# Optimization experiments

Hardware: AMD Instinct MI355X
Metric: run time of the kernel (lower is better)

## Reference

```python
import jax, jax.numpy as jnp
import numpy as np

N_NODES = 100000
N_EDGES = 1600000
DIM = 64
BN_EPS = 1e-5


def setup_inputs() -> dict:
    key = jax.random.key(0)
    ks = jax.random.split(key, 6)
    x = jax.random.normal(ks[0], (N_NODES, DIM), dtype=jnp.float32)
    edge_index = jax.random.randint(ks[1], (2, N_EDGES), 0, N_NODES, dtype=jnp.int32)
    W = jax.random.normal(ks[2], (DIM, DIM), dtype=jnp.float32) / np.sqrt(DIM)
    b = jax.random.normal(ks[3], (DIM,), dtype=jnp.float32) * 0.01
    gamma = jnp.ones((DIM,), dtype=jnp.float32)
    beta = jnp.zeros((DIM,), dtype=jnp.float32)
    return {"x": x, "edge_index": edge_index, "W": W, "b": b, "gamma": gamma, "beta": beta}


def reference(x, edge_index, W, b, gamma, beta):
    n = x.shape[0]
    src, dst = edge_index[0], edge_index[1]
    # GCNConv adds self loops
    loop = jnp.arange(n, dtype=edge_index.dtype)
    src = jnp.concatenate([src, loop])
    dst = jnp.concatenate([dst, loop])
    # symmetric degree normalization: D^-1/2 (A+I) D^-1/2
    deg = jax.ops.segment_sum(jnp.ones(src.shape[0], x.dtype), dst, num_segments=n)
    dinv = jnp.where(deg > 0, jax.lax.rsqrt(deg), 0.0)
    norm = dinv[src] * dinv[dst]  # [E+N]
    h = x @ W  # [N, D] transform before aggregation (GCN order)
    msg = h[src] * norm[:, None]  # gather + scale
    out = jax.ops.segment_sum(msg, dst, num_segments=n) + b  # scatter-add
    # BatchNorm1d (training mode: batch statistics, biased variance)
    mean = jnp.mean(out, axis=0)
    var = jnp.mean(jnp.square(out - mean), axis=0)
    out = (out - mean) * jax.lax.rsqrt(var + BN_EPS) * gamma + beta
    # ReLU; dropout is identity in eval mode
    return jax.nn.relu(out)
```

## Files before the change

kernel.cpp:

```cpp
#include <hip/hip_runtime.h>

#define N_NODES 100000
#define N_EDGES 1600000
#define DIM 64
#define BN_EPS 1e-5f

#define BNODES 128
#define NBUCK ((N_NODES + BNODES - 1) / BNODES)
#define CAP_RAW 2560
#define CAP_OUT 3584
#define TILE 4096
#define ABLK ((N_EDGES + TILE - 1) / TILE)
#define DUMMY N_NODES

#define GBLK 6250

typedef __bf16 bf16x8 __attribute__((ext_vector_type(8)));
typedef float floatx4 __attribute__((ext_vector_type(4)));

static __device__ __forceinline__ unsigned short f2bf(float f) {
    unsigned u = __float_as_uint(f);
    u = (u + 0x7FFFu + ((u >> 16) & 1u)) >> 16;
    return (unsigned short)u;
}
static __device__ __forceinline__ float bf2f(unsigned short h) {
    return __uint_as_float(((unsigned)h) << 16);
}

__global__ void __launch_bounds__(1024)
passA_kernel(const int* __restrict__ src, const int* __restrict__ dst,
             int* __restrict__ cur, unsigned int* __restrict__ entries, int E) {
    __shared__ int hist[NBUCK];
    __shared__ int lbase[NBUCK];
    int t = threadIdx.x;
    if (t < NBUCK) hist[t] = 0;
    __syncthreads();

    int e0   = blockIdx.x * TILE;
    int eend = min(e0 + TILE, E);

    int dreg[4], sreg[4], ne = 0;
    for (int e = e0 + t; e < eend; e += 1024) {
        dreg[ne] = dst[e];
        sreg[ne] = src[e];
        atomicAdd(&hist[dreg[ne] >> 7], 1);
        ++ne;
    }
    __syncthreads();
    if (t < NBUCK) {
        int ii = t + (blockIdx.x * 331) % NBUCK;
        if (ii >= NBUCK) ii -= NBUCK;
        int c = hist[ii];
        lbase[ii] = (c > 0) ? atomicAdd(&cur[ii], c) : 0;
        hist[ii] = 0;
    }
    __syncthreads();
    for (int k = 0; k < ne; ++k) {
        int s = sreg[k];
        int d = dreg[k];
        int b = d >> 7;
        int r = atomicAdd(&hist[b], 1);
        int pos = lbase[b] + r;
        if (pos < CAP_RAW)
            entries[(size_t)b * CAP_OUT + pos] = ((unsigned)s << 7) | (unsigned)(d & 127);
    }
}

__global__ void passB1_kernel(unsigned int* __restrict__ entries, const int* __restrict__ cur,
                              int* __restrict__ rowbeg, int* __restrict__ rowend,
                              float* __restrict__ dinv, int N) {
    __shared__ unsigned int raw[CAP_RAW];
    __shared__ int hist[BNODES];
    __shared__ int sbuf[BNODES];
    __shared__ int startx[BNODES];
    __shared__ int cursor[BNODES];
    int bucket = blockIdx.x;
    int t = threadIdx.x;
    int node0 = bucket * BNODES;
    int nn = min(BNODES, N - node0);
    int cnt = min(cur[bucket], CAP_RAW);
    unsigned int* eb = entries + (size_t)bucket * CAP_OUT;

    if (t < BNODES) hist[t] = 0;
    __syncthreads();
    for (int i = t; i < cnt; i += 256) {
        unsigned int e = eb[i];
        raw[i] = e;
        atomicAdd(&hist[e & 127], 1);
    }
    __syncthreads();
    int pdeg_t = 0;
    if (t < BNODES) { pdeg_t = (hist[t] + 7) & ~7; sbuf[t] = pdeg_t; }
    __syncthreads();
    for (int off = 1; off < BNODES; off <<= 1) {
        int add = (t < BNODES && t >= off) ? sbuf[t - off] : 0;
        __syncthreads();
        if (t < BNODES) sbuf[t] += add;
        __syncthreads();
    }
    if (t < BNODES) {
        int ex = sbuf[t] - pdeg_t;
        startx[t] = ex;
        cursor[t] = ex;
    }
    __syncthreads();
    for (int i = t; i < cnt; i += 256) {
        unsigned int e = raw[i];
        int d = e & 127;
        int p = atomicAdd(&cursor[d], 1);
        eb[p] = e >> 7;
    }
    if (t < nn) {
        int dg  = hist[t];
        int pdg = (dg + 7) & ~7;
        int base = startx[t];
        for (int k = dg; k < pdg; ++k) eb[base + k] = DUMMY;
        int gbase = bucket * CAP_OUT + base;
        rowbeg[node0 + t] = gbase;
        rowend[node0 + t] = gbase + pdg;
        dinv[node0 + t]   = rsqrtf((float)(dg + 1));
    }
}

__global__ void __launch_bounds__(256)
gemm_kernel(const float* __restrict__ x, const float* __restrict__ W,
            const float* __restrict__ dinv, unsigned short* __restrict__ hb, int N) {
    int wave  = (blockIdx.x * blockDim.x + threadIdx.x) >> 6;
    int lane  = threadIdx.x & 63;
    int m     = lane & 15;
    int quad  = lane >> 4;

    bf16x8 bfrag[2][4];
#pragma unroll
    for (int c = 0; c < 2; ++c)
#pragma unroll
        for (int nt = 0; nt < 4; ++nt) {
            bf16x8 f;
#pragma unroll
            for (int j = 0; j < 8; ++j) {
                int k = c * 32 + quad * 8 + j;
                f[j] = (__bf16)W[k * DIM + nt * 16 + m];
            }
            bfrag[c][nt] = f;
        }

    int nchunks    = N >> 4;
    int totalwaves = (gridDim.x * blockDim.x) >> 6;
    for (int chunk = wave; chunk < nchunks; chunk += totalwaves) {
        int row0 = chunk * 16;
        const float* xr = x + (size_t)(row0 + m) * DIM;
        bf16x8 afrag[2];
#pragma unroll
        for (int c = 0; c < 2; ++c) {
            float4 lo = *(const float4*)(xr + c * 32 + quad * 8);
            float4 hi = *(const float4*)(xr + c * 32 + quad * 8 + 4);
            bf16x8 f;
            f[0] = (__bf16)lo.x; f[1] = (__bf16)lo.y; f[2] = (__bf16)lo.z; f[3] = (__bf16)lo.w;
            f[4] = (__bf16)hi.x; f[5] = (__bf16)hi.y; f[6] = (__bf16)hi.z; f[7] = (__bf16)hi.w;
            afrag[c] = f;
        }
        float dv[4];
#pragma unroll
        for (int r = 0; r < 4; ++r) dv[r] = dinv[row0 + quad * 4 + r];
#pragma unroll
        for (int nt = 0; nt < 4; ++nt) {
            floatx4 acc = {0.f, 0.f, 0.f, 0.f};
            acc = __builtin_amdgcn_mfma_f32_16x16x32_bf16(afrag[0], bfrag[0][nt], acc, 0, 0, 0);
            acc = __builtin_amdgcn_mfma_f32_16x16x32_bf16(afrag[1], bfrag[1][nt], acc, 0, 0, 0);
#pragma unroll
            for (int r = 0; r < 4; ++r) {
                int row = row0 + quad * 4 + r;
                hb[(size_t)row * DIM + nt * 16 + m] = f2bf(acc[r] * dv[r]);
            }
        }
    }
}

__global__ void __launch_bounds__(256)
gather_kernel(const int* __restrict__ rowbeg, const int* __restrict__ rowend,
              const unsigned int* __restrict__ srt, const unsigned short* __restrict__ hb,
              const float* __restrict__ dinv, float* __restrict__ out,
              float* __restrict__ partial, int N) {
    __shared__ float red[2][4][64];
    int lane = threadIdx.x & 63;
    int wv   = threadIdx.x >> 6;
    int g    = blockIdx.x * 4 + wv;
    int n0   = g << 2;
    float s_sum = 0.f, s_sq = 0.f;

    if (n0 < N) {
        int beg = __builtin_amdgcn_readfirstlane(rowbeg[n0]);
        int s1  = __builtin_amdgcn_readfirstlane(rowbeg[n0 + 1]);
        int s2  = __builtin_amdgcn_readfirstlane(rowbeg[n0 + 2]);
        int s3  = __builtin_amdgcn_readfirstlane(rowbeg[n0 + 3]);
        int end = __builtin_amdgcn_readfirstlane(rowend[n0 + 3]);
        float acc0 = 0.f, acc1 = 0.f, acc2 = 0.f, acc3 = 0.f;

        for (int base = beg; base < end; base += 64) {
            int idx = base + lane;
            unsigned int sv = (idx < end) ? srt[idx] : 0u;
            int cn = min(64, end - base);
            for (int j = 0; j < cn; j += 8) {
                int p0 = base + j;
                int k = (p0 >= s1) + (p0 >= s2) + (p0 >= s3);
                float v[8];
#pragma unroll
                for (int u = 0; u < 8; ++u) {
                    unsigned int s = (unsigned)__shfl((int)sv, j + u, 64);
                    v[u] = bf2f(hb[(size_t)s * DIM + lane]);
                }
                float csum = ((v[0] + v[1]) + (v[2] + v[3])) +
                             ((v[4] + v[5]) + (v[6] + v[7]));
                acc0 += (k == 0) ? csum : 0.f;
                acc1 += (k == 1) ? csum : 0.f;
                acc2 += (k == 2) ? csum : 0.f;
                acc3 += (k == 3) ? csum : 0.f;
            }
        }

        float v0 = (acc0 + bf2f(hb[(size_t)(n0 + 0) * DIM + lane])) * dinv[n0 + 0];
        float v1 = (acc1 + bf2f(hb[(size_t)(n0 + 1) * DIM + lane])) * dinv[n0 + 1];
        float v2 = (acc2 + bf2f(hb[(size_t)(n0 + 2) * DIM + lane])) * dinv[n0 + 2];
        float v3 = (acc3 + bf2f(hb[(size_t)(n0 + 3) * DIM + lane])) * dinv[n0 + 3];
        out[(size_t)(n0 + 0) * DIM + lane] = v0;
        out[(size_t)(n0 + 1) * DIM + lane] = v1;
        out[(size_t)(n0 + 2) * DIM + lane] = v2;
        out[(size_t)(n0 + 3) * DIM + lane] = v3;
        s_sum = ((v0 + v1) + (v2 + v3));
        s_sq  = ((v0 * v0 + v1 * v1) + (v2 * v2 + v3 * v3));
    }

    red[0][wv][lane] = s_sum;
    red[1][wv][lane] = s_sq;
    __syncthreads();
    if (threadIdx.x < 64) {
        int c = threadIdx.x;
        partial[(size_t)blockIdx.x * 128 + c] =
            red[0][0][c] + red[0][1][c] + red[0][2][c] + red[0][3][c];
        partial[(size_t)blockIdx.x * 128 + 64 + c] =
            red[1][0][c] + red[1][1][c] + red[1][2][c] + red[1][3][c];
    }
}

__global__ void reduce2_kernel(const float* __restrict__ partial, float* __restrict__ gstat) {
    __shared__ float buf[256];
    int t = threadIdx.x;
    int col = t & 127;
    int half = t >> 7;
    int r0 = blockIdx.x * 125;
    float acc = 0.f;
    for (int r = r0 + half; r < r0 + 125; r += 2)
        acc += partial[(size_t)r * 128 + col];
    buf[t] = acc;
    __syncthreads();
    if (t < 128) atomicAdd(&gstat[t], buf[t] + buf[t + 128]);
}

__global__ void bn_finalize_kernel(const float* __restrict__ gsum, const float* __restrict__ gsumsq,
                                   const float* __restrict__ gamma, const float* __restrict__ beta,
                                   float* __restrict__ scale, float* __restrict__ shift, int N) {
    int c = threadIdx.x;
    float invN = 1.0f / (float)N;
    float mean = gsum[c] * invN;
    float var  = gsumsq[c] * invN - mean * mean;
    float sc   = gamma[c] * rsqrtf(var + BN_EPS);
    scale[c] = sc;
    shift[c] = beta[c] - mean * sc;
}

__global__ void bn_apply_kernel(float4* __restrict__ out, const float* __restrict__ scale,
                                const float* __restrict__ shift, int total4) {
    int i = blockIdx.x * blockDim.x + threadIdx.x;
    if (i >= total4) return;
    int c = (i * 4) & 63;
    float4 v = out[i];
    float a0 = fmaf(v.x, scale[c],     shift[c]);
    float a1 = fmaf(v.y, scale[c + 1], shift[c + 1]);
    float a2 = fmaf(v.z, scale[c + 2], shift[c + 2]);
    float a3 = fmaf(v.w, scale[c + 3], shift[c + 3]);
    v.x = a0 > 0.f ? a0 : 0.f;
    v.y = a1 > 0.f ? a1 : 0.f;
    v.z = a2 > 0.f ? a2 : 0.f;
    v.w = a3 > 0.f ? a3 : 0.f;
    out[i] = v;
}

extern "C" void kernel_launch(void* const* d_in, const int* in_sizes, int n_in,
                              void* d_out, int out_size, void* d_ws, size_t ws_size,
                              hipStream_t stream) {
    const float* x     = (const float*)d_in[0];
    const int*   eidx  = (const int*)d_in[1];
    const float* W     = (const float*)d_in[2];
    const float* gamma = (const float*)d_in[4];
    const float* beta  = (const float*)d_in[5];
    float* out = (float*)d_out;

    const int N = N_NODES;
    const int E = N_EDGES;
    const int total = N * DIM;

    const int* src = eidx;
    const int* dst = eidx + E;

    unsigned short* hb = (unsigned short*)d_ws;
    float* dinv      = (float*)(hb + (size_t)(N + 1) * DIM);
    int*   rowbeg    = (int*)(dinv + N);
    int*   rowend    = rowbeg + N;
    int*   cur       = rowend + N;
    float* gsum      = (float*)(cur + NBUCK);
    float* gsumsq    = gsum + 64;
    float* scale     = gsumsq + 64;
    float* shift     = scale + 64;
    unsigned int* entries = (unsigned int*)(shift + 64);
    float* partial   = (float*)(entries + (size_t)NBUCK * CAP_OUT);

    hipMemsetAsync(cur, 0, (size_t)(NBUCK + 128) * sizeof(int), stream);
    hipMemsetAsync(hb + (size_t)N * DIM, 0, DIM * sizeof(unsigned short), stream);

    passA_kernel<<<ABLK, 1024, 0, stream>>>(src, dst, cur, entries, E);

    passB1_kernel<<<NBUCK, 256, 0, stream>>>(entries, cur, rowbeg, rowend, dinv, N);

    gemm_kernel<<<512, 256, 0, stream>>>(x, W, dinv, hb, N);

    gather_kernel<<<GBLK, 256, 0, stream>>>(rowbeg, rowend, entries, hb, dinv, out, partial, N);

    reduce2_kernel<<<50, 256, 0, stream>>>(partial, gsum);

    bn_finalize_kernel<<<1, 64, 0, stream>>>(gsum, gsumsq, gamma, beta, scale, shift, N);
    bn_apply_kernel<<<(total / 4 + 255) / 256, 256, 0, stream>>>((float4*)out, scale, shift, total / 4);
}
```

Measured before the change: 197.4 us.

## Fuse GEMM into CSR build kernel and merge BN finalize into apply

Moves the MFMA transform x@W (scaled by dinv) into the per-bucket CSR build kernel, so each 128-node bucket computes its own rows of hb right after computing dinv, reading dinv from shared memory. BN finalize is folded into the apply kernel, with every block recomputing scale and shift into shared memory. The two memsets become one by placing the zero row used for padding entries in the zeroed scratch region. This removes two launches and one memset, at the cost of reloading W per bucket block and repeating the BN finalize math in each block.

```diff
diff --git a/kernel.cpp b/kernel.cpp
--- a/kernel.cpp
+++ b/kernel.cpp
@@ -11,7 +11,6 @@
 #define CAP_OUT 3584
 #define TILE 4096
 #define ABLK ((N_EDGES + TILE - 1) / TILE)
-#define DUMMY N_NODES
 
 #define GBLK 6250
 
@@ -66,14 +65,18 @@
     }
 }
 
-__global__ void passB1_kernel(unsigned int* __restrict__ entries, const int* __restrict__ cur,
-                              int* __restrict__ rowbeg, int* __restrict__ rowend,
-                              float* __restrict__ dinv, int N) {
+__global__ void __launch_bounds__(256)
+build_kernel(unsigned int* __restrict__ entries, const int* __restrict__ cur,
+             int* __restrict__ rowbeg, int* __restrict__ rowend,
+             float* __restrict__ dinv,
+             const float* __restrict__ x, const float* __restrict__ W,
+             unsigned short* __restrict__ hb, int dummyIdx, int N) {
     __shared__ unsigned int raw[CAP_RAW];
     __shared__ int hist[BNODES];
     __shared__ int sbuf[BNODES];
     __shared__ int startx[BNODES];
     __shared__ int cursor[BNODES];
+    __shared__ float sdinv[BNODES];
     int bucket = blockIdx.x;
     int t = threadIdx.x;
     int node0 = bucket * BNODES;
@@ -114,63 +117,60 @@
         int dg  = hist[t];
         int pdg = (dg + 7) & ~7;
         int base = startx[t];
-        for (int k = dg; k < pdg; ++k) eb[base + k] = DUMMY;
+        for (int k = dg; k < pdg; ++k) eb[base + k] = (unsigned)dummyIdx;
         int gbase = bucket * CAP_OUT + base;
         rowbeg[node0 + t] = gbase;
         rowend[node0 + t] = gbase + pdg;
-        dinv[node0 + t]   = rsqrtf((float)(dg + 1));
-    }
-}
-
-__global__ void __launch_bounds__(256)
-gemm_kernel(const float* __restrict__ x, const float* __restrict__ W,
-            const float* __restrict__ dinv, unsigned short* __restrict__ hb, int N) {
-    int wave  = (blockIdx.x * blockDim.x + threadIdx.x) >> 6;
-    int lane  = threadIdx.x & 63;
-    int m     = lane & 15;
-    int quad  = lane >> 4;
-
-    bf16x8 bfrag[2][4];
-#pragma unroll
-    for (int c = 0; c < 2; ++c)
-#pragma unroll
-        for (int nt = 0; nt < 4; ++nt) {
-            bf16x8 f;
-#pragma unroll
-            for (int j = 0; j < 8; ++j) {
-                int k = c * 32 + quad * 8 + j;
-                f[j] = (__bf16)W[k * DIM + nt * 16 + m];
+        float di = rsqrtf((float)(dg + 1));
+        dinv[node0 + t] = di;
+        sdinv[t] = di;
+    }
+    __syncthreads();
+
+    int lane = t & 63, wv = t >> 6;
+    int m = lane & 15, quad = lane >> 4;
+    int nchunk = nn >> 4;
+    if (wv < nchunk || nchunk == 8) {
+        bf16x8 bfrag[2][4];
+#pragma unroll
+        for (int c = 0; c < 2; ++c)
+#pragma unroll
+            for (int nt = 0; nt < 4; ++nt) {
+                bf16x8 f;
+#pragma unroll
+                for (int j = 0; j < 8; ++j) {
+                    int k = c * 32 + quad * 8 + j;
+                    f[j] = (__bf16)W[k * DIM + nt * 16 + m];
+                }
+                bfrag[c][nt] = f;
             }
-            bfrag[c][nt] = f;
-        }
-
-    int nchunks    = N >> 4;
-    int totalwaves = (gridDim.x * blockDim.x) >> 6;
-    for (int chunk = wave; chunk < nchunks; chunk += totalwaves) {
-        int row0 = chunk * 16;
-        const float* xr = x + (size_t)(row0 + m) * DIM;
-        bf16x8 afrag[2];
-#pragma unroll
-        for (int c = 0; c < 2; ++c) {
-            float4 lo = *(const float4*)(xr + c * 32 + quad * 8);
-            float4 hi = *(const float4*)(xr + c * 32 + quad * 8 + 4);
-            bf16x8 f;
-            f[0] = (__bf16)lo.x; f[1] = (__bf16)lo.y; f[2] = (__bf16)lo.z; f[3] = (__bf16)lo.w;
-            f[4] = (__bf16)hi.x; f[5] = (__bf16)hi.y; f[6] = (__bf16)hi.z; f[7] = (__bf16)hi.w;
-            afrag[c] = f;
-        }
-        float dv[4];
-#pragma unroll
-        for (int r = 0; r < 4; ++r) dv[r] = dinv[row0 + quad * 4 + r];
-#pragma unroll
-        for (int nt = 0; nt < 4; ++nt) {
-            floatx4 acc = {0.f, 0.f, 0.f, 0.f};
-            acc = __builtin_amdgcn_mfma_f32_16x16x32_bf16(afrag[0], bfrag[0][nt], acc, 0, 0, 0);
-            acc = __builtin_amdgcn_mfma_f32_16x16x32_bf16(afrag[1], bfrag[1][nt], acc, 0, 0, 0);
-#pragma unroll
-            for (int r = 0; r < 4; ++r) {
-                int row = row0 + quad * 4 + r;
-                hb[(size_t)row * DIM + nt * 16 + m] = f2bf(acc[r] * dv[r]);
+        for (int c2 = wv; c2 < nchunk; c2 += 4) {
+            int lrow0 = c2 * 16;
+            int row0 = node0 + lrow0;
+            const float* xr = x + (size_t)(row0 + m) * DIM;
+            bf16x8 afrag[2];
+#pragma unroll
+            for (int c = 0; c < 2; ++c) {
+                float4 lo = *(const float4*)(xr + c * 32 + quad * 8);
+                float4 hi = *(const float4*)(xr + c * 32 + quad * 8 + 4);
+                bf16x8 f;
+                f[0] = (__bf16)lo.x; f[1] = (__bf16)lo.y; f[2] = (__bf16)lo.z; f[3] = (__bf16)lo.w;
+                f[4] = (__bf16)hi.x; f[5] = (__bf16)hi.y; f[6] = (__bf16)hi.z; f[7] = (__bf16)hi.w;
+                afrag[c] = f;
+            }
+            float dv[4];
+#pragma unroll
+            for (int r = 0; r < 4; ++r) dv[r] = sdinv[lrow0 + quad * 4 + r];
+#pragma unroll
+            for (int nt = 0; nt < 4; ++nt) {
+                floatx4 acc = {0.f, 0.f, 0.f, 0.f};
+                acc = __builtin_amdgcn_mfma_f32_16x16x32_bf16(afrag[0], bfrag[0][nt], acc, 0, 0, 0);
+                acc = __builtin_amdgcn_mfma_f32_16x16x32_bf16(afrag[1], bfrag[1][nt], acc, 0, 0, 0);
+#pragma unroll
+                for (int r = 0; r < 4; ++r) {
+                    int row = row0 + quad * 4 + r;
+                    hb[(size_t)row * DIM + nt * 16 + m] = f2bf(acc[r] * dv[r]);
+                }
             }
         }
     }
@@ -256,21 +256,23 @@
     if (t < 128) atomicAdd(&gstat[t], buf[t] + buf[t + 128]);
 }
 
-__global__ void bn_finalize_kernel(const float* __restrict__ gsum, const float* __restrict__ gsumsq,
-                                   const float* __restrict__ gamma, const float* __restrict__ beta,
-                                   float* __restrict__ scale, float* __restrict__ shift, int N) {
-    int c = threadIdx.x;
-    float invN = 1.0f / (float)N;
-    float mean = gsum[c] * invN;
-    float var  = gsumsq[c] * invN - mean * mean;
-    float sc   = gamma[c] * rsqrtf(var + BN_EPS);
-    scale[c] = sc;
-    shift[c] = beta[c] - mean * sc;
-}
-
-__global__ void bn_apply_kernel(float4* __restrict__ out, const float* __restrict__ scale,
-                                const float* __restrict__ shift, int total4) {
-    int i = blockIdx.x * blockDim.x + threadIdx.x;
+__global__ void __launch_bounds__(256)
+finish_kernel(float4* __restrict__ out, const float* __restrict__ gstat,
+              const float* __restrict__ gamma, const float* __restrict__ beta,
+              int total4, int N) {
+    __shared__ float scale[64];
+    __shared__ float shift[64];
+    int t = threadIdx.x;
+    if (t < 64) {
+        float invN = 1.0f / (float)N;
+        float mean = gstat[t] * invN;
+        float var  = gstat[64 + t] * invN - mean * mean;
+        float sc   = gamma[t] * rsqrtf(var + BN_EPS);
+        scale[t] = sc;
+        shift[t] = beta[t] - mean * sc;
+    }
+    __syncthreads();
+    int i = blockIdx.x * blockDim.x + t;
     if (i >= total4) return;
     int c = (i * 4) & 63;
     float4 v = out[i];
@@ -296,37 +298,42 @@
     float* out = (float*)d_out;
 
     const int N = N_NODES;
-    const int E = N_EDGES;
     const int total = N * DIM;
 
     const int* src = eidx;
-    const int* dst = eidx + E;
-
-    unsigned short* hb = (unsigned short*)d_ws;
-    float* dinv      = (float*)(hb + (size_t)(N + 1) * DIM);
-    int*   rowbeg    = (int*)(dinv + N);
-    int*   rowend    = rowbeg + N;
-    int*   cur       = rowend + N;
-    float* gsum      = (float*)(cur + NBUCK);
-    float* gsumsq    = gsum + 64;
-    float* scale     = gsumsq + 64;
-    float* shift     = scale + 64;
-    unsigned int* entries = (unsigned int*)(shift + 64);
-    float* partial   = (float*)(entries + (size_t)NBUCK * CAP_OUT);
-
-    hipMemsetAsync(cur, 0, (size_t)(NBUCK + 128) * sizeof(int), stream);
-    hipMemsetAsync(hb + (size_t)N * DIM, 0, DIM * sizeof(unsigned short), stream);
-
-    passA_kernel<<<ABLK, 1024, 0, stream>>>(src, dst, cur, entries, E);
-
-    passB1_kernel<<<NBUCK, 256, 0, stream>>>(entries, cur, rowbeg, rowend, dinv, N);
-
-    gemm_kernel<<<512, 256, 0, stream>>>(x, W, dinv, hb, N);
+    const int* dst = eidx + N_EDGES;
+
+    char* ws = (char*)d_ws;
+    size_t off_hb      = 0;
+    size_t off_dinv    = off_hb + (size_t)N * DIM * 2;
+    size_t off_rowbeg  = off_dinv + (size_t)N * 4;
+    size_t off_rowend  = off_rowbeg + (size_t)N * 4;
+    size_t off_entries = off_rowend + (size_t)N * 4;
+    size_t off_partial = off_entries + (size_t)NBUCK * CAP_OUT * 4;
+    size_t off_z       = off_partial + (size_t)GBLK * 128 * 4;
+
+    unsigned short* hb    = (unsigned short*)(ws + off_hb);
+    float*          dinv  = (float*)(ws + off_dinv);
+    int*            rowbeg = (int*)(ws + off_rowbeg);
+    int*            rowend = (int*)(ws + off_rowend);
+    unsigned int*   entries = (unsigned int*)(ws + off_entries);
+    float*          partial = (float*)(ws + off_partial);
+    int*   cur   = (int*)(ws + off_z + 128);
+    float* gstat = (float*)(cur + NBUCK);
+    int dummyIdx = (int)(off_z / (DIM * 2));
+
+    size_t zbytes = 128 + (size_t)NBUCK * 4 + 512;
+    hipMemsetAsync(ws + off_z, 0, zbytes, stream);
+
+    passA_kernel<<<ABLK, 1024, 0, stream>>>(src, dst, cur, entries, N_EDGES);
+
+    build_kernel<<<NBUCK, 256, 0, stream>>>(entries, cur, rowbeg, rowend, dinv,
+                                            x, W, hb, dummyIdx, N);
 
     gather_kernel<<<GBLK, 256, 0, stream>>>(rowbeg, rowend, entries, hb, dinv, out, partial, N);
 
-    reduce2_kernel<<<50, 256, 0, stream>>>(partial, gsum);
-
-    bn_finalize_kernel<<<1, 64, 0, stream>>>(gsum, gsumsq, gamma, beta, scale, shift, N);
-    bn_apply_kernel<<<(total / 4 + 255) / 256, 256, 0, stream>>>((float4*)out, scale, shift, total / 4);
-}
+    reduce2_kernel<<<50, 256, 0, stream>>>(partial, gstat);
+
+    finish_kernel<<<(total / 4 + 255) / 256, 256, 0, stream>>>((float4*)out, gstat,
+                                                               gamma, beta, total / 4, N);
+}
```

Result: no change. 197.7 us (+0.2%).
